# Performance work log

Hardware: AMD Instinct MI355X
Metric: run time of the kernel (lower is better)

The kernel has to match this reference:

```python
import jax, jax.numpy as jnp
import numpy as np
from jax import lax

N, T, V, E, H, D, B = 16384, 16, 10000, 256, 256, 512, 128


def setup_inputs() -> dict:
    key = jax.random.key(0)
    ks = jax.random.split(key, 12)
    tok = jax.random.randint(ks[0], (N, T), 1, V)
    lens = jax.random.randint(ks[1], (N,), 4, T + 1)
    tok = jnp.where(jnp.arange(T)[None, :] < lens[:, None], tok, 0)  # pad_id = 0
    ast_path_len = jnp.full((B,), N // B, dtype=jnp.int32)  # 128 paths per sample
    u = lambda k, s: jax.random.uniform(k, s, jnp.float32, -0.1, 0.1)
    emb = u(ks[2], (V, E)).at[0].set(0.0)  # padding_idx=0 row zeroed
    return {
        "ast_path": tok,
        "ast_path_len": ast_path_len,
        "emb": emb,
        "W_ih_f": u(ks[3], (4 * H, E)), "W_hh_f": u(ks[4], (4 * H, H)), "b_f": u(ks[5], (4 * H,)),
        "W_ih_b": u(ks[6], (4 * H, E)), "W_hh_b": u(ks[7], (4 * H, H)), "b_b": u(ks[8], (4 * H,)),
        "W_lin": u(ks[9], (D, 2 * H)), "b_lin": jnp.zeros((D,), jnp.float32),
    }


def _lstm_final_h(x_tm, lens, W_ih, W_hh, b, reverse):
    # x_tm: [T, N, E]; returns final hidden state [N, H] honoring per-seq length
    n = x_tm.shape[1]
    h0 = jnp.zeros((n, H), x_tm.dtype)

    def step(carry, xt):
        h, c = carry
        x, t = xt
        gates = x @ W_ih.T + h @ W_hh.T + b  # [N, 4H]
        i, f, g, o = jnp.split(gates, 4, axis=-1)
        c_new = jax.nn.sigmoid(f) * c + jax.nn.sigmoid(i) * jnp.tanh(g)
        h_new = jax.nn.sigmoid(o) * jnp.tanh(c_new)
        m = (t < lens)[:, None]  # packed-sequence semantics: frozen past length
        return (jnp.where(m, h_new, h), jnp.where(m, c_new, c)), None

    (h, _), _ = lax.scan(step, (h0, h0), (x_tm, jnp.arange(x_tm.shape[0])), reverse=reverse)
    return h


def reference(ast_path, ast_path_len, emb, W_ih_f, W_hh_f, b_f, W_ih_b, W_hh_b, b_b, W_lin, b_lin):
    lens = (ast_path != 0).sum(axis=-1)  # pad_id = 0
    x = emb[ast_path]                     # [N, T, E]; dropout is identity at eval
    x_tm = jnp.swapaxes(x, 0, 1)          # [T, N, E]
    h_fwd = _lstm_final_h(x_tm, lens, W_ih_f, W_hh_f, b_f, reverse=False)
    h_bwd = _lstm_final_h(x_tm, lens, W_ih_b, W_hh_b, b_b, reverse=True)
    h_n = jnp.concatenate([h_fwd, h_bwd], axis=1)        # [N, 2H]
    repr_ = h_n @ W_lin.T + b_lin                         # [N, D]
    # segment-mean pooling over path groups (replaces the Python loop)
    n_paths = repr_.shape[0]
    seg_ids = jnp.repeat(jnp.arange(ast_path_len.shape[0]), ast_path_len,
                         total_repeat_length=n_paths)
    sums = jax.ops.segment_sum(repr_, seg_ids, num_segments=ast_path_len.shape[0])
    pooled = sums / ast_path_len[:, None].astype(repr_.dtype)  # [B, D]
    norm = jnp.sqrt(jnp.sum(pooled * pooled, axis=-1, keepdims=True))
    return pooled / jnp.maximum(norm, 1e-5)
```

## Files before the change

### kernel.cpp

```cpp
#include <hip/hip_runtime.h>
#include <stdint.h>

#define N_SEQ 16384
#define T_LEN 16
#define E_DIM 256
#define H_DIM 256
#define K_DIM 512
#define B_SAMP 128
#define V_SIZE 10000

typedef __bf16 bf16x8 __attribute__((ext_vector_type(8)));
typedef float  f32x4  __attribute__((ext_vector_type(4)));

__device__ __forceinline__ unsigned short f2bf(float x) {
  unsigned int u = __float_as_uint(x);
  u = (u + 0x7fffu + ((u >> 16) & 1u)) >> 16;
  return (unsigned short)u;
}
__device__ __forceinline__ float bf2f(unsigned short v) {
  return __uint_as_float(((unsigned int)v) << 16);
}
__device__ __forceinline__ float sigmoidf_(float x) {
  return 1.0f / (1.0f + __expf(-x));
}
__device__ __forceinline__ void glds16(const void* g, const void* l) {
  __builtin_amdgcn_global_load_lds(
      (const __attribute__((address_space(1))) unsigned int*)g,
      (__attribute__((address_space(3))) unsigned int*)l, 16, 0, 0);
}


__global__ __launch_bounds__(256) void k_lens(const int* __restrict__ tok, int* __restrict__ lens) {
  int n = blockIdx.x * 256 + threadIdx.x;
  const int* r = tok + n * T_LEN;
  int c = 0;
#pragma unroll
  for (int t = 0; t < T_LEN; ++t) c += (r[t] != 0);
  lens[n] = c;
}

__global__ __launch_bounds__(256) void k_embcvt(const float* __restrict__ emb, unsigned short* __restrict__ out) {
  int i = blockIdx.x * 256 + threadIdx.x;
  out[i] = f2bf(emb[i]);
}

__global__ __launch_bounds__(256) void k_wprep(const float* __restrict__ Wih_f, const float* __restrict__ Whh_f,
                                               const float* __restrict__ Wih_b, const float* __restrict__ Whh_b,
                                               unsigned short* __restrict__ wpt_f, unsigned short* __restrict__ wpt_b) {
  int id = blockIdx.x * 256 + threadIdx.x;
  int dir = id >> 19;
  int rem = id & ((1 << 19) - 1);
  int p = rem >> 9;
  int k = rem & 511;
  int nb = p >> 8, wc = (p >> 6) & 3, q = (p >> 4) & 3, jj = p & 15;
  int r = q * 256 + nb * 64 + wc * 16 + jj;
  const float* Wih = dir ? Wih_b : Wih_f;
  const float* Whh = dir ? Whh_b : Whh_f;
  float v = (k < 256) ? Wih[r * 256 + k] : Whh[r * 256 + (k - 256)];
  unsigned short* o = dir ? wpt_b : wpt_f;
  o[p * 512 + k] = f2bf(v);
}


__global__ __launch_bounds__(512, 4)
void k_step(const unsigned short* __restrict__ embbf, const int* __restrict__ tok,
            const int* __restrict__ lens,
            const unsigned short* __restrict__ wpt_f, const unsigned short* __restrict__ wpt_b,
            const float* __restrict__ bias_f, const float* __restrict__ bias_b,
            const unsigned short* __restrict__ hr_f, unsigned short* __restrict__ hw_f,
            const unsigned short* __restrict__ hr_b, unsigned short* __restrict__ hw_b,
            float* __restrict__ c_f, float* __restrict__ c_b,
            int s) {
  const int dir = blockIdx.y;
  const int t = dir ? (T_LEN - 1 - s) : s;
  const unsigned short* wpt = dir ? wpt_b : wpt_f;
  const float* bias = dir ? bias_b : bias_f;
  const unsigned short* hr = dir ? hr_b : hr_f;
  unsigned short* hw = dir ? hw_b : hw_f;
  float* cc = dir ? c_b : c_f;

  const int mblk = blockIdx.x >> 2;
  const int nblk = blockIdx.x & 3;
  const int m0 = mblk * 128;

  __shared__ __align__(128) unsigned char ldsA[128 * 128];
  __shared__ __align__(128) unsigned char ldsB[256 * 128];

  const int tid = threadIdx.x;
  const int lane = tid & 63;
  const int w = tid >> 6;
  const int wr = w >> 2;
  const int wc = w & 3;

  const int l8 = lane >> 3;
  const int l7 = lane & 7;
  const int arow0 = 16 * w + l8;
  const int arow1 = arow0 + 8;
  const int ach0 = l7 ^ (arow0 & 7);
  const int ach1 = l7 ^ (arow1 & 7);
  const unsigned aoffE0 = (unsigned)tok[(m0 + arow0) * T_LEN + t] * E_DIM + ach0 * 8;
  const unsigned aoffE1 = (unsigned)tok[(m0 + arow1) * T_LEN + t] * E_DIM + ach1 * 8;
  const unsigned aoffH0 = (unsigned)(m0 + arow0) * H_DIM + ach0 * 8;
  const unsigned aoffH1 = (unsigned)(m0 + arow1) * H_DIM + ach1 * 8;
  unsigned boff[4];
#pragma unroll
  for (int j = 0; j < 4; ++j) {
    const int brow = 32 * w + 8 * j + l8;
    const int bch = l7 ^ (brow & 7);
    boff[j] = (unsigned)(nblk * 256 + brow) * K_DIM + bch * 8;
  }

  f32x4 acc[4][4] = {};
  const int frow = lane & 15;
  const int fkq = lane >> 4;

  for (int kt = 0; kt < 8; ++kt) {
    const int k0 = kt * 64;
    if (kt < 4) {
      glds16(embbf + aoffE0 + k0, &ldsA[(16 * w) * 128]);
      glds16(embbf + aoffE1 + k0, &ldsA[(16 * w + 8) * 128]);
    } else {
      glds16(hr + aoffH0 + (k0 - E_DIM), &ldsA[(16 * w) * 128]);
      glds16(hr + aoffH1 + (k0 - E_DIM), &ldsA[(16 * w + 8) * 128]);
    }
#pragma unroll
    for (int j = 0; j < 4; ++j)
      glds16(wpt + boff[j] + k0, &ldsB[(32 * w + 8 * j) * 128]);
    __syncthreads();
#pragma unroll
    for (int ksub = 0; ksub < 2; ++ksub) {
      bf16x8 av[4], bv[4];
#pragma unroll
      for (int fr = 0; fr < 4; ++fr) {
        const int row = wr * 64 + fr * 16 + frow;
        const int ch = (ksub * 4 + fkq) ^ (row & 7);
        av[fr] = *(const bf16x8*)&ldsA[row * 128 + ch * 16];
      }
#pragma unroll
      for (int fc = 0; fc < 4; ++fc) {
        const int row = wc * 64 + fc * 16 + frow;
        const int ch = (ksub * 4 + fkq) ^ (row & 7);
        bv[fc] = *(const bf16x8*)&ldsB[row * 128 + ch * 16];
      }
#pragma unroll
      for (int fr = 0; fr < 4; ++fr)
#pragma unroll
        for (int fc = 0; fc < 4; ++fc)
          acc[fr][fc] = __builtin_amdgcn_mfma_f32_16x16x32_bf16(av[fr], bv[fc], acc[fr][fc], 0, 0, 0);
    }
    __syncthreads();
  }

  const int j = nblk * 64 + wc * 16 + frow;
  const float bi = bias[j], bfv = bias[256 + j], bg = bias[512 + j], bo = bias[768 + j];
#pragma unroll
  for (int fr = 0; fr < 4; ++fr) {
    const int nbase = m0 + wr * 64 + fr * 16 + fkq * 4;
    const int4 ln4 = *(const int4*)&lens[nbase];
    const f32x4 gi = acc[fr][0], gf = acc[fr][1], gg = acc[fr][2], go = acc[fr][3];
#pragma unroll
    for (int r = 0; r < 4; ++r) {
      const int n = nbase + r;
      const int ln = (r == 0) ? ln4.x : (r == 1) ? ln4.y : (r == 2) ? ln4.z : ln4.w;
      const size_t idx = (size_t)n * H_DIM + j;
      if (t < ln) {
        float iv = sigmoidf_(gi[r] + bi);
        float fv = sigmoidf_(gf[r] + bfv);
        float gv = tanhf(gg[r] + bg);
        float ov = sigmoidf_(go[r] + bo);
        float cn = fv * cc[idx] + iv * gv;
        cc[idx] = cn;
        hw[idx] = f2bf(ov * tanhf(cn));
      } else {
        hw[idx] = hr[idx];
      }
    }
  }
}


__global__ __launch_bounds__(256) void k_pool(const unsigned short* __restrict__ hf,
                                              const unsigned short* __restrict__ hb,
                                              const int* __restrict__ plen,
                                              float* __restrict__ pooled) {
  const int b = blockIdx.x, tid = threadIdx.x;
  int start = 0;
  for (int i = 0; i < b; ++i) start += plen[i];
  const int cnt = plen[b];
  float s0 = 0.f, s1 = 0.f;
  for (int r = 0; r < cnt; ++r) {
    s0 += bf2f(hf[(size_t)(start + r) * H_DIM + tid]);
    s1 += bf2f(hb[(size_t)(start + r) * H_DIM + tid]);
  }
  float inv = 1.0f / (float)cnt;
  pooled[b * 512 + tid] = s0 * inv;
  pooled[b * 512 + H_DIM + tid] = s1 * inv;
}


__global__ __launch_bounds__(256) void k_final(const float* __restrict__ pooled,
                                               const float* __restrict__ W,
                                               const float* __restrict__ bl,
                                               float* __restrict__ out) {
  const int b = blockIdx.x, tid = threadIdx.x;
  __shared__ float pv[512];
  __shared__ float pre[512];
  __shared__ float red[4];
  pv[tid] = pooled[b * 512 + tid];
  pv[tid + 256] = pooled[b * 512 + 256 + tid];
  __syncthreads();
#pragma unroll
  for (int half = 0; half < 2; ++half) {
    const int dd = tid + half * 256;
    const f32x4* wr = (const f32x4*)(W + (size_t)dd * 512);
    const f32x4* pvv = (const f32x4*)pv;
    float s = bl[dd];
#pragma unroll 4
    for (int k4 = 0; k4 < 128; ++k4) {
      f32x4 wv = wr[k4], xv = pvv[k4];
      s += wv[0] * xv[0] + wv[1] * xv[1] + wv[2] * xv[2] + wv[3] * xv[3];
    }
    pre[dd] = s;
  }
  __syncthreads();
  float ss = pre[tid] * pre[tid] + pre[tid + 256] * pre[tid + 256];
#pragma unroll
  for (int off = 32; off > 0; off >>= 1) ss += __shfl_down(ss, off, 64);
  if ((tid & 63) == 0) red[tid >> 6] = ss;
  __syncthreads();
  float tot = red[0] + red[1] + red[2] + red[3];
  float scale = 1.0f / fmaxf(sqrtf(tot), 1e-5f);
  out[b * 512 + tid] = pre[tid] * scale;
  out[b * 512 + 256 + tid] = pre[tid + 256] * scale;
}


extern "C" void kernel_launch(void* const* d_in, const int* in_sizes, int n_in,
                              void* d_out, int out_size, void* d_ws, size_t ws_size,
                              hipStream_t stream) {
  const int* tok    = (const int*)d_in[0];
  const int* plen   = (const int*)d_in[1];
  const float* emb  = (const float*)d_in[2];
  const float* Wih_f = (const float*)d_in[3];
  const float* Whh_f = (const float*)d_in[4];
  const float* b_f   = (const float*)d_in[5];
  const float* Wih_b = (const float*)d_in[6];
  const float* Whh_b = (const float*)d_in[7];
  const float* b_b   = (const float*)d_in[8];
  const float* Wlin  = (const float*)d_in[9];
  const float* blin  = (const float*)d_in[10];
  float* out = (float*)d_out;

  char* ws = (char*)d_ws;
  size_t off = 0;
  auto alloc = [&](size_t bytes) {
    void* p = ws + off;
    off = (off + bytes + 255) & ~(size_t)255;
    return p;
  };
  unsigned short* embbf = (unsigned short*)alloc((size_t)V_SIZE * E_DIM * 2);
  unsigned short* wptf  = (unsigned short*)alloc((size_t)1024 * K_DIM * 2);
  unsigned short* wptb  = (unsigned short*)alloc((size_t)1024 * K_DIM * 2);
  int* lens             = (int*)alloc((size_t)N_SEQ * 4);
  unsigned short* h0f   = (unsigned short*)alloc((size_t)N_SEQ * H_DIM * 2);
  unsigned short* h1f   = (unsigned short*)alloc((size_t)N_SEQ * H_DIM * 2);
  unsigned short* h0b   = (unsigned short*)alloc((size_t)N_SEQ * H_DIM * 2);
  unsigned short* h1b   = (unsigned short*)alloc((size_t)N_SEQ * H_DIM * 2);
  float* cf             = (float*)alloc((size_t)N_SEQ * H_DIM * 4);
  float* cb             = (float*)alloc((size_t)N_SEQ * H_DIM * 4);
  float* pooled         = (float*)alloc((size_t)B_SAMP * 512 * 4);

  hipMemsetAsync(h0f, 0, (size_t)N_SEQ * H_DIM * 2, stream);
  hipMemsetAsync(h0b, 0, (size_t)N_SEQ * H_DIM * 2, stream);
  hipMemsetAsync(cf, 0, (size_t)N_SEQ * H_DIM * 4, stream);
  hipMemsetAsync(cb, 0, (size_t)N_SEQ * H_DIM * 4, stream);

  k_lens<<<N_SEQ / 256, 256, 0, stream>>>(tok, lens);
  k_embcvt<<<(V_SIZE * E_DIM) / 256, 256, 0, stream>>>(emb, embbf);
  k_wprep<<<(2 * 1024 * K_DIM) / 256, 256, 0, stream>>>(Wih_f, Whh_f, Wih_b, Whh_b, wptf, wptb);

  dim3 grid(512, 2);
  for (int s = 0; s < T_LEN; ++s) {
    const unsigned short* hrf = (s & 1) ? h1f : h0f;
    unsigned short* hwf       = (s & 1) ? h0f : h1f;
    const unsigned short* hrb = (s & 1) ? h1b : h0b;
    unsigned short* hwb       = (s & 1) ? h0b : h1b;
    k_step<<<grid, 512, 0, stream>>>(embbf, tok, lens, wptf, wptb, b_f, b_b,
                                     hrf, hwf, hrb, hwb, cf, cb, s);
  }
  k_pool<<<B_SAMP, 256, 0, stream>>>(h0f, h0b, plen, pooled);
  k_final<<<B_SAMP, 256, 0, stream>>>(pooled, Wlin, blin, out);
}
```

Measured before the change: 1.015 ms.

## Sort sequences by length and skip fully inactive row blocks per step

Adds a histogram, offset and scatter pass that orders sequences by descending length, giving a permutation, its inverse and permuted lengths. Each LSTM step now exits early for 128-row blocks whose rows are all past their length, so masked timesteps no longer cost GEMM work. Hidden and cell state live in sorted order, embedding gather goes through the permutation, and pooling maps back through the inverse permutation. The per-step count keeps one extra trailing step so both ping-pong hidden buffers hold the final state, and both buffers are zeroed up front. The cost is a few extra tiny launches plus an indirect gather in the pooling kernel.

```diff
diff --git a/kernel.cpp b/kernel.cpp
--- a/kernel.cpp
+++ b/kernel.cpp
@@ -37,6 +37,38 @@
 #pragma unroll
   for (int t = 0; t < T_LEN; ++t) c += (r[t] != 0);
   lens[n] = c;
+}
+
+__global__ __launch_bounds__(256) void k_hist(const int* __restrict__ lens, int* __restrict__ hist) {
+  __shared__ int lh[17];
+  if (threadIdx.x < 17) lh[threadIdx.x] = 0;
+  __syncthreads();
+  atomicAdd(&lh[lens[blockIdx.x * 256 + threadIdx.x]], 1);
+  __syncthreads();
+  if (threadIdx.x < 17) atomicAdd(&hist[threadIdx.x], lh[threadIdx.x]);
+}
+
+__global__ void k_offsets(const int* __restrict__ hist, int* __restrict__ cursor, int* __restrict__ cnts) {
+  if (threadIdx.x == 0) {
+    int off = 0;
+    for (int l = 16; l >= 0; --l) { cursor[l] = off; off += hist[l]; }
+    for (int t = 0; t < 16; ++t) {
+      int c = 0;
+      for (int l = t; l <= 16; ++l) c += hist[l];
+      cnts[t] = c;
+    }
+  }
+}
+
+__global__ __launch_bounds__(256) void k_scatter(const int* __restrict__ lens, int* __restrict__ cursor,
+                                                 int* __restrict__ perm, int* __restrict__ pinv,
+                                                 int* __restrict__ plens) {
+  int n = blockIdx.x * 256 + threadIdx.x;
+  int l = lens[n];
+  int pos = atomicAdd(&cursor[l], 1);
+  perm[pos] = n;
+  pinv[n] = pos;
+  plens[pos] = l;
 }
 
 __global__ __launch_bounds__(256) void k_embcvt(const float* __restrict__ emb, unsigned short* __restrict__ out) {
@@ -64,7 +96,8 @@
 
 __global__ __launch_bounds__(512, 4)
 void k_step(const unsigned short* __restrict__ embbf, const int* __restrict__ tok,
-            const int* __restrict__ lens,
+            const int* __restrict__ perm, const int* __restrict__ plens,
+            const int* __restrict__ cnts,
             const unsigned short* __restrict__ wpt_f, const unsigned short* __restrict__ wpt_b,
             const float* __restrict__ bias_f, const float* __restrict__ bias_b,
             const unsigned short* __restrict__ hr_f, unsigned short* __restrict__ hw_f,
@@ -73,15 +106,17 @@
             int s) {
   const int dir = blockIdx.y;
   const int t = dir ? (T_LEN - 1 - s) : s;
+  const int mblk = blockIdx.x >> 2;
+  const int m0 = mblk * 128;
+  const int cnt = cnts[dir ? (15 - s) : s];
+  if (m0 >= cnt) return;
+
+  const int nblk = blockIdx.x & 3;
   const unsigned short* wpt = dir ? wpt_b : wpt_f;
   const float* bias = dir ? bias_b : bias_f;
   const unsigned short* hr = dir ? hr_b : hr_f;
   unsigned short* hw = dir ? hw_b : hw_f;
   float* cc = dir ? c_b : c_f;
-
-  const int mblk = blockIdx.x >> 2;
-  const int nblk = blockIdx.x & 3;
-  const int m0 = mblk * 128;
 
   __shared__ __align__(128) unsigned char ldsA[128 * 128];
   __shared__ __align__(128) unsigned char ldsB[256 * 128];
@@ -98,8 +133,10 @@
   const int arow1 = arow0 + 8;
   const int ach0 = l7 ^ (arow0 & 7);
   const int ach1 = l7 ^ (arow1 & 7);
-  const unsigned aoffE0 = (unsigned)tok[(m0 + arow0) * T_LEN + t] * E_DIM + ach0 * 8;
-  const unsigned aoffE1 = (unsigned)tok[(m0 + arow1) * T_LEN + t] * E_DIM + ach1 * 8;
+  const int pn0 = perm[m0 + arow0];
+  const int pn1 = perm[m0 + arow1];
+  const unsigned aoffE0 = (unsigned)tok[pn0 * T_LEN + t] * E_DIM + ach0 * 8;
+  const unsigned aoffE1 = (unsigned)tok[pn1 * T_LEN + t] * E_DIM + ach1 * 8;
   const unsigned aoffH0 = (unsigned)(m0 + arow0) * H_DIM + ach0 * 8;
   const unsigned aoffH1 = (unsigned)(m0 + arow1) * H_DIM + ach1 * 8;
   unsigned boff[4];
@@ -156,7 +193,7 @@
 #pragma unroll
   for (int fr = 0; fr < 4; ++fr) {
     const int nbase = m0 + wr * 64 + fr * 16 + fkq * 4;
-    const int4 ln4 = *(const int4*)&lens[nbase];
+    const int4 ln4 = *(const int4*)&plens[nbase];
     const f32x4 gi = acc[fr][0], gf = acc[fr][1], gg = acc[fr][2], go = acc[fr][3];
 #pragma unroll
     for (int r = 0; r < 4; ++r) {
@@ -181,6 +218,7 @@
 
 __global__ __launch_bounds__(256) void k_pool(const unsigned short* __restrict__ hf,
                                               const unsigned short* __restrict__ hb,
+                                              const int* __restrict__ pinv,
                                               const int* __restrict__ plen,
                                               float* __restrict__ pooled) {
   const int b = blockIdx.x, tid = threadIdx.x;
@@ -189,8 +227,9 @@
   const int cnt = plen[b];
   float s0 = 0.f, s1 = 0.f;
   for (int r = 0; r < cnt; ++r) {
-    s0 += bf2f(hf[(size_t)(start + r) * H_DIM + tid]);
-    s1 += bf2f(hb[(size_t)(start + r) * H_DIM + tid]);
+    const size_t pr = (size_t)pinv[start + r];
+    s0 += bf2f(hf[pr * H_DIM + tid]);
+    s1 += bf2f(hb[pr * H_DIM + tid]);
   }
   float inv = 1.0f / (float)cnt;
   pooled[b * 512 + tid] = s0 * inv;
@@ -262,6 +301,12 @@
   unsigned short* wptf  = (unsigned short*)alloc((size_t)1024 * K_DIM * 2);
   unsigned short* wptb  = (unsigned short*)alloc((size_t)1024 * K_DIM * 2);
   int* lens             = (int*)alloc((size_t)N_SEQ * 4);
+  int* perm             = (int*)alloc((size_t)N_SEQ * 4);
+  int* pinv             = (int*)alloc((size_t)N_SEQ * 4);
+  int* plens            = (int*)alloc((size_t)N_SEQ * 4);
+  int* hist             = (int*)alloc(17 * 4);
+  int* cursor           = (int*)alloc(17 * 4);
+  int* cnts             = (int*)alloc(16 * 4);
   unsigned short* h0f   = (unsigned short*)alloc((size_t)N_SEQ * H_DIM * 2);
   unsigned short* h1f   = (unsigned short*)alloc((size_t)N_SEQ * H_DIM * 2);
   unsigned short* h0b   = (unsigned short*)alloc((size_t)N_SEQ * H_DIM * 2);
@@ -270,12 +315,18 @@
   float* cb             = (float*)alloc((size_t)N_SEQ * H_DIM * 4);
   float* pooled         = (float*)alloc((size_t)B_SAMP * 512 * 4);
 
+  hipMemsetAsync(hist, 0, 17 * 4, stream);
   hipMemsetAsync(h0f, 0, (size_t)N_SEQ * H_DIM * 2, stream);
   hipMemsetAsync(h0b, 0, (size_t)N_SEQ * H_DIM * 2, stream);
+  hipMemsetAsync(h1f, 0, (size_t)N_SEQ * H_DIM * 2, stream);
+  hipMemsetAsync(h1b, 0, (size_t)N_SEQ * H_DIM * 2, stream);
   hipMemsetAsync(cf, 0, (size_t)N_SEQ * H_DIM * 4, stream);
   hipMemsetAsync(cb, 0, (size_t)N_SEQ * H_DIM * 4, stream);
 
   k_lens<<<N_SEQ / 256, 256, 0, stream>>>(tok, lens);
+  k_hist<<<N_SEQ / 256, 256, 0, stream>>>(lens, hist);
+  k_offsets<<<1, 64, 0, stream>>>(hist, cursor, cnts);
+  k_scatter<<<N_SEQ / 256, 256, 0, stream>>>(lens, cursor, perm, pinv, plens);
   k_embcvt<<<(V_SIZE * E_DIM) / 256, 256, 0, stream>>>(emb, embbf);
   k_wprep<<<(2 * 1024 * K_DIM) / 256, 256, 0, stream>>>(Wih_f, Whh_f, Wih_b, Whh_b, wptf, wptb);
 
@@ -285,9 +336,9 @@
     unsigned short* hwf       = (s & 1) ? h0f : h1f;
     const unsigned short* hrb = (s & 1) ? h1b : h0b;
     unsigned short* hwb       = (s & 1) ? h0b : h1b;
-    k_step<<<grid, 512, 0, stream>>>(embbf, tok, lens, wptf, wptb, b_f, b_b,
+    k_step<<<grid, 512, 0, stream>>>(embbf, tok, perm, plens, cnts, wptf, wptb, b_f, b_b,
                                      hrf, hwf, hrb, hwb, cf, cb, s);
   }
-  k_pool<<<B_SAMP, 256, 0, stream>>>(h0f, h0b, plen, pooled);
+  k_pool<<<B_SAMP, 256, 0, stream>>>(h0f, h0b, pinv, plen, pooled);
   k_final<<<B_SAMP, 256, 0, stream>>>(pooled, Wlin, blin, out);
 }
```

Result: faster. 943.6 us (-7.0%).
